# Kernel optimization log

Measured on AMD Instinct MI355X. Metric: run time of the kernel, lower is better.

## Reference

```python
import jax, jax.numpy as jnp
import numpy as np

ROUTING_ITERS = 3


def _squash(x, axis=-1):
    # sum_sq/(1+sum_sq) * x/sqrt(sum_sq), faithful to the torch squash
    sum_sq = jnp.sum(x * x, axis=axis, keepdims=True)
    return sum_sq / (1.0 + sum_sq) * x / jnp.sqrt(sum_sq)


def setup_inputs() -> dict:
    key = jax.random.key(0)
    k1, k2 = jax.random.split(key)
    B, I, O, Din, Dout = 256, 1152, 10, 8, 16
    x = jax.random.normal(k1, (B, I, Din), dtype=jnp.float32)
    W = jax.random.normal(k2, (I, O, Din, Dout), dtype=jnp.float32)
    return {"x": x, "W": W}


def reference(x, W):
    # x: [B, I, Din], W: [I, O, Din, Dout]
    I, O, Din, Dout = W.shape
    # u_hat = x @ W per (capsule_in, capsule_out): [B, I, O, Dout]
    u_hat = jnp.einsum('bid,iode->bioe', x, W)
    b = jnp.zeros((I, O), dtype=x.dtype)  # coupling logits, shared over batch
    v = None
    for _ in range(ROUTING_ITERS):
        c = jax.nn.softmax(b, axis=1)                    # softmax over out capsules
        s = jnp.einsum('bioe,io->boe', u_hat, c)         # weighted sum over in caps
        v = _squash(s, axis=-1)                          # [B, O, Dout]
        # agreement, averaged over batch (torch does .mean(dim=0))
        agree = jnp.einsum('bioe,boe->bio', u_hat, v).mean(axis=0)  # [I, O]
        b = b + agree
    # torch returns v.squeeze(1).transpose(2,3) -> [B, O, Dout, 1]
    return v[..., None]
```

## Files before the change

### kernel.cpp

```cpp
#include <hip/hip_runtime.h>
#include <math.h>

#define B    256
#define I    1152
#define O    10
#define DIN  8
#define DOUT 16
#define OE   160
#define XROW 9216
#define WROW 1280
#define PSPLIT 72
#define CHUNK  16
#define SI     8

typedef __attribute__((ext_vector_type(8))) short short8;
typedef __attribute__((ext_vector_type(4))) float floatx4;

__device__ __forceinline__ unsigned short f2bf(float f) {
    unsigned u = __builtin_bit_cast(unsigned, f);
    u += 0x7fffu + ((u >> 16) & 1u);
    return (unsigned short)(u >> 16);
}
__device__ __forceinline__ float bf2f(unsigned short h) {
    unsigned u = ((unsigned)h) << 16;
    return __builtin_bit_cast(float, u);
}

__global__ __launch_bounds__(256) void xsplit_kernel(
    const float* __restrict__ x,
    unsigned short* __restrict__ xh, unsigned short* __restrict__ xl)
{
    int g = blockIdx.x * 256 + threadIdx.x;
    float4 v = ((const float4*)x)[g];
    ushort4 h, l;
    h.x = f2bf(v.x); l.x = f2bf(v.x - bf2f(h.x));
    h.y = f2bf(v.y); l.y = f2bf(v.y - bf2f(h.y));
    h.z = f2bf(v.z); l.z = f2bf(v.z - bf2f(h.z));
    h.w = f2bf(v.w); l.w = f2bf(v.w - bf2f(h.w));
    ((ushort4*)xh)[g] = h;
    ((ushort4*)xl)[g] = l;
}

__global__ __launch_bounds__(256) void spart_mfma(
    const unsigned short* __restrict__ xh, const unsigned short* __restrict__ xl,
    const float* __restrict__ W, const float* __restrict__ c,
    float* __restrict__ sp, int first)
{
    __shared__ unsigned short Wh[80 * 64], Wl[80 * 64];
    __shared__ unsigned short Xh[128 * 64], Xl[128 * 64];

    int bid = blockIdx.x;
    int ic  = bid >> 2;
    int mb  = (bid >> 1) & 1;
    int nb  = bid & 1;
    int b0  = mb * 128;
    int oe0 = nb * 80;
    int o0  = nb * 5;
    int i0  = ic * CHUNK;

    int t    = threadIdx.x;
    int w    = t >> 6;
    int lane = t & 63;
    int l15  = lane & 15;
    int q    = lane >> 4;

    floatx4 acc[2][5];
#pragma unroll
    for (int mt = 0; mt < 2; ++mt)
#pragma unroll
        for (int nt = 0; nt < 5; ++nt) acc[mt][nt] = (floatx4)(0.f);

#pragma unroll
    for (int round = 0; round < CHUNK / SI; ++round) {
        int si0 = i0 + round * SI;
        if (round) __syncthreads();

#pragma unroll
        for (int r = 0; r < 3; ++r) {
            int p = t + 256 * r;
            if (p < 640) {
                int oeL = p % 80;
                int iL  = p / 80;
                int o   = o0 + (oeL >> 4);
                int e   = oeL & 15;
                const float* wp = W + (size_t)(si0 + iL) * WROW + o * (DIN * DOUT) + e;
                float cv = first ? 0.1f : c[(si0 + iL) * O + o];
                short8 hv, lv;
#pragma unroll
                for (int d = 0; d < 8; ++d) {
                    float wv = wp[d * DOUT] * cv;
                    unsigned short h = f2bf(wv);
                    hv[d] = (short)h;
                    lv[d] = (short)f2bf(wv - bf2f(h));
                }
                int off = oeL * 64 + ((iL ^ (oeL & 7)) << 3);
                *(short8*)(Wh + off) = hv;
                *(short8*)(Wl + off) = lv;
            }
        }
#pragma unroll
        for (int r = 0; r < 4; ++r) {
            int cg  = t + 256 * r;
            int row = cg >> 3;
            int ch  = cg & 7;
            size_t goff = (size_t)(b0 + row) * XROW + (size_t)si0 * 8 + (ch << 3);
            short8 vh = *(const short8*)(xh + goff);
            short8 vl = *(const short8*)(xl + goff);
            int off = row * 64 + ((ch ^ (row & 7)) << 3);
            *(short8*)(Xh + off) = vh;
            *(short8*)(Xl + off) = vl;
        }
        __syncthreads();

#pragma unroll
        for (int ks = 0; ks < 2; ++ks) {
            short8 ah[2], al[2];
#pragma unroll
            for (int mt = 0; mt < 2; ++mt) {
                int rm  = w * 32 + mt * 16 + l15;
                int off = rm * 64 + ((((ks << 2) + q) ^ (rm & 7)) << 3);
                ah[mt] = *(const short8*)(Xh + off);
                al[mt] = *(const short8*)(Xl + off);
            }
#pragma unroll
            for (int nt = 0; nt < 5; ++nt) {
                int rn  = nt * 16 + l15;
                int off = rn * 64 + ((((ks << 2) + q) ^ (rn & 7)) << 3);
                short8 bh = *(const short8*)(Wh + off);
                short8 bl = *(const short8*)(Wl + off);
#pragma unroll
                for (int mt = 0; mt < 2; ++mt) {
                    acc[mt][nt] = __builtin_amdgcn_mfma_f32_16x16x32_bf16(ah[mt], bh, acc[mt][nt], 0, 0, 0);
                    acc[mt][nt] = __builtin_amdgcn_mfma_f32_16x16x32_bf16(ah[mt], bl, acc[mt][nt], 0, 0, 0);
                    acc[mt][nt] = __builtin_amdgcn_mfma_f32_16x16x32_bf16(al[mt], bh, acc[mt][nt], 0, 0, 0);
                }
            }
        }
    }

    float* base = sp + (size_t)ic * (B * OE);
#pragma unroll
    for (int mt = 0; mt < 2; ++mt) {
        int row0 = b0 + w * 32 + mt * 16 + q * 4;
#pragma unroll
        for (int nt = 0; nt < 5; ++nt) {
            int col = oe0 + nt * 16 + l15;
#pragma unroll
            for (int reg = 0; reg < 4; ++reg)
                base[(row0 + reg) * OE + col] = acc[mt][nt][reg];
        }
    }
}

__global__ __launch_bounds__(256) void vred_kernel(
    const float* __restrict__ sp, float* __restrict__ dst)
{
    int g = blockIdx.x * 256 + threadIdx.x;
    float s = 0.f;
#pragma unroll 4
    for (int ic = 0; ic < PSPLIT; ++ic) s += sp[(size_t)ic * (B * OE) + g];

    float ss = s * s;
    ss += __shfl_xor(ss, 1, 16);
    ss += __shfl_xor(ss, 2, 16);
    ss += __shfl_xor(ss, 4, 16);
    ss += __shfl_xor(ss, 8, 16);
    float f = sqrtf(ss) / (1.f + ss);
    dst[g] = s * f;
}

__global__ __launch_bounds__(320) void agree_kernel(
    const float* __restrict__ x, const float* __restrict__ W,
    const float* __restrict__ v, float* __restrict__ blog,
    float* __restrict__ c, int first)
{
    int i  = blockIdx.x;
    int t  = threadIdx.x;
    int dg = (t >= OE) ? 1 : 0;
    int oe = t - dg * OE;

    __shared__ float4 Xl[B][2];
    __shared__ float  G[DIN * OE];
    __shared__ float  brow[O];

#pragma unroll
    for (int k = 0; k < 2; ++k) {
        int idx = t + 320 * k;
        if (idx < 512) {
            int r = idx >> 1;
            int h = idx & 1;
            Xl[r][h] = *(const float4*)(x + (size_t)r * XROW + i * DIN + h * 4);
        }
    }
    __syncthreads();

    float a0 = 0.f, a1 = 0.f, a2 = 0.f, a3 = 0.f;
    const float* vp = v + oe;
#pragma unroll 8
    for (int bb = 0; bb < B; ++bb) {
        float  vv = vp[bb * OE];
        float4 xq = Xl[bb][dg];
        a0 = fmaf(xq.x, vv, a0);
        a1 = fmaf(xq.y, vv, a1);
        a2 = fmaf(xq.z, vv, a2);
        a3 = fmaf(xq.w, vv, a3);
    }

    int d0 = dg * 4;
    G[(d0 + 0) * OE + oe] = a0;
    G[(d0 + 1) * OE + oe] = a1;
    G[(d0 + 2) * OE + oe] = a2;
    G[(d0 + 3) * OE + oe] = a3;
    __syncthreads();

    if (t < OE) {
        int o = t >> 4;
        const float* wr = W + (size_t)i * WROW + o * (DIN * DOUT) + (t & 15);
        float p = 0.f;
#pragma unroll
        for (int d = 0; d < DIN; ++d) p = fmaf(wr[d * DOUT], G[d * OE + t], p);
        p += __shfl_xor(p, 8, 16);
        p += __shfl_xor(p, 4, 16);
        p += __shfl_xor(p, 2, 16);
        p += __shfl_xor(p, 1, 16);
        if ((t & 15) == 0) {
            float bo = first ? 0.f : blog[i * O + o];
            bo += p * (1.f / (float)B);
            blog[i * O + o] = bo;
            brow[o] = bo;
        }
    }
    __syncthreads();

    if (t == 0) {
        float m = brow[0];
#pragma unroll
        for (int o = 1; o < O; ++o) m = fmaxf(m, brow[o]);
        float ex[O];
        float sum = 0.f;
#pragma unroll
        for (int o = 0; o < O; ++o) { ex[o] = __expf(brow[o] - m); sum += ex[o]; }
        float inv = 1.f / sum;
#pragma unroll
        for (int o = 0; o < O; ++o) c[i * O + o] = ex[o] * inv;
    }
}

extern "C" void kernel_launch(void* const* d_in, const int* in_sizes, int n_in,
                              void* d_out, int out_size, void* d_ws, size_t ws_size,
                              hipStream_t stream)
{
    const float* x = (const float*)d_in[0];
    const float* W = (const float*)d_in[1];
    float* out = (float*)d_out;

    unsigned short* xh = (unsigned short*)d_ws;
    unsigned short* xl = xh + (size_t)B * XROW;
    float* blog = (float*)(xl + (size_t)B * XROW);
    float* cbuf = blog + I * O;
    float* vbuf = cbuf + I * O;
    float* sp   = vbuf + B * OE;

    xsplit_kernel<<<(B * XROW) / (256 * 4), 256, 0, stream>>>(x, xh, xl);

    dim3 gs(4 * PSPLIT), bs(256);
    spart_mfma<<<gs, bs, 0, stream>>>(xh, xl, W, cbuf, sp, 1);
    vred_kernel<<<160, 256, 0, stream>>>(sp, vbuf);
    agree_kernel<<<I, 320, 0, stream>>>(x, W, vbuf, blog, cbuf, 1);
    spart_mfma<<<gs, bs, 0, stream>>>(xh, xl, W, cbuf, sp, 0);
    vred_kernel<<<160, 256, 0, stream>>>(sp, vbuf);
    agree_kernel<<<I, 320, 0, stream>>>(x, W, vbuf, blog, cbuf, 0);
    spart_mfma<<<gs, bs, 0, stream>>>(xh, xl, W, cbuf, sp, 0);
    vred_kernel<<<160, 256, 0, stream>>>(sp, out);
}
```

Measured before the change: 165.8 us.

## Split x into bf16 inside MFMA kernel and pre-transpose W for vector loads

Drops the separate x split kernel and its bf16 hi/lo workspace. Each wave now loads its MFMA A fragments directly from fp32 x in registers, which also removes the X shared-memory tiles. A new prep kernel transposes W once per call into an [i][oe][d] layout, so the spart and agree kernels can read 8 contiguous floats instead of strided scalars. The trade-offs are redundant x conversion across the three routing iterations and the N-split blocks, plus an extra W transpose pass. The vred loop unroll is also raised.

New measurement: 159.7 us. 1.04x faster.

```diff
diff --git a/kernel.cpp b/kernel.cpp
--- a/kernel.cpp
+++ b/kernel.cpp
@@ -13,6 +13,8 @@
 #define CHUNK  16
 #define SI     8
 
+#define WPREP_BLOCKS ((I * OE) / 256)
+
 typedef __attribute__((ext_vector_type(8))) short short8;
 typedef __attribute__((ext_vector_type(4))) float floatx4;
 
@@ -26,28 +28,43 @@
     return __builtin_bit_cast(float, u);
 }
 
-__global__ __launch_bounds__(256) void xsplit_kernel(
+__device__ __forceinline__ void split8(const float* __restrict__ xp,
+                                       short8& h8, short8& l8)
+{
+    float4 v0 = *(const float4*)xp;
+    float4 v1 = *(const float4*)(xp + 4);
+    float v[8] = {v0.x, v0.y, v0.z, v0.w, v1.x, v1.y, v1.z, v1.w};
+#pragma unroll
+    for (int d = 0; d < 8; ++d) {
+        unsigned short h = f2bf(v[d]);
+        h8[d] = (short)h;
+        l8[d] = (short)f2bf(v[d] - bf2f(h));
+    }
+}
+
+__global__ __launch_bounds__(256) void wprep_kernel(
+    const float* __restrict__ W, float* __restrict__ Wt)
+{
+    int g  = blockIdx.x * 256 + threadIdx.x;
+    int i  = g / OE;
+    int oe = g - i * OE;
+    int o  = oe >> 4;
+    int e  = oe & 15;
+    const float* wp = W + (size_t)i * WROW + o * (DIN * DOUT) + e;
+    float4 a, b;
+    a.x = wp[0 * DOUT]; a.y = wp[1 * DOUT]; a.z = wp[2 * DOUT]; a.w = wp[3 * DOUT];
+    b.x = wp[4 * DOUT]; b.y = wp[5 * DOUT]; b.z = wp[6 * DOUT]; b.w = wp[7 * DOUT];
+    float4* dst = (float4*)(Wt + (size_t)g * 8);
+    dst[0] = a;
+    dst[1] = b;
+}
+
+__global__ __launch_bounds__(256) void spart_mfma(
     const float* __restrict__ x,
-    unsigned short* __restrict__ xh, unsigned short* __restrict__ xl)
-{
-    int g = blockIdx.x * 256 + threadIdx.x;
-    float4 v = ((const float4*)x)[g];
-    ushort4 h, l;
-    h.x = f2bf(v.x); l.x = f2bf(v.x - bf2f(h.x));
-    h.y = f2bf(v.y); l.y = f2bf(v.y - bf2f(h.y));
-    h.z = f2bf(v.z); l.z = f2bf(v.z - bf2f(h.z));
-    h.w = f2bf(v.w); l.w = f2bf(v.w - bf2f(h.w));
-    ((ushort4*)xh)[g] = h;
-    ((ushort4*)xl)[g] = l;
-}
-
-__global__ __launch_bounds__(256) void spart_mfma(
-    const unsigned short* __restrict__ xh, const unsigned short* __restrict__ xl,
-    const float* __restrict__ W, const float* __restrict__ c,
+    const float* __restrict__ Wt, const float* __restrict__ c,
     float* __restrict__ sp, int first)
 {
     __shared__ unsigned short Wh[80 * 64], Wl[80 * 64];
-    __shared__ unsigned short Xh[128 * 64], Xl[128 * 64];
 
     int bid = blockIdx.x;
     int ic  = bid >> 2;
@@ -55,7 +72,6 @@
     int nb  = bid & 1;
     int b0  = mb * 128;
     int oe0 = nb * 80;
-    int o0  = nb * 5;
     int i0  = ic * CHUNK;
 
     int t    = threadIdx.x;
@@ -75,53 +91,45 @@
         int si0 = i0 + round * SI;
         if (round) __syncthreads();
 
+        short8 ah[2][2], al[2][2];
+#pragma unroll
+        for (int ks = 0; ks < 2; ++ks)
+#pragma unroll
+            for (int mt = 0; mt < 2; ++mt) {
+                const float* xp = x + (size_t)(b0 + w * 32 + mt * 16 + l15) * XROW
+                                + (size_t)si0 * 8 + (ks << 5) + (q << 3);
+                split8(xp, ah[ks][mt], al[ks][mt]);
+            }
+
 #pragma unroll
         for (int r = 0; r < 3; ++r) {
             int p = t + 256 * r;
             if (p < 640) {
                 int oeL = p % 80;
                 int iL  = p / 80;
-                int o   = o0 + (oeL >> 4);
-                int e   = oeL & 15;
-                const float* wp = W + (size_t)(si0 + iL) * WROW + o * (DIN * DOUT) + e;
+                int o   = (oe0 + oeL) >> 4;
+                const float* wp = Wt + ((size_t)(si0 + iL) * OE + oe0 + oeL) * 8;
                 float cv = first ? 0.1f : c[(si0 + iL) * O + o];
+                float4 w0 = *(const float4*)wp;
+                float4 w1 = *(const float4*)(wp + 4);
+                float wv[8] = {w0.x, w0.y, w0.z, w0.w, w1.x, w1.y, w1.z, w1.w};
                 short8 hv, lv;
 #pragma unroll
                 for (int d = 0; d < 8; ++d) {
-                    float wv = wp[d * DOUT] * cv;
-                    unsigned short h = f2bf(wv);
+                    float s = wv[d] * cv;
+                    unsigned short h = f2bf(s);
                     hv[d] = (short)h;
-                    lv[d] = (short)f2bf(wv - bf2f(h));
+                    lv[d] = (short)f2bf(s - bf2f(h));
                 }
                 int off = oeL * 64 + ((iL ^ (oeL & 7)) << 3);
                 *(short8*)(Wh + off) = hv;
                 *(short8*)(Wl + off) = lv;
             }
         }
-#pragma unroll
-        for (int r = 0; r < 4; ++r) {
-            int cg  = t + 256 * r;
-            int row = cg >> 3;
-            int ch  = cg & 7;
-            size_t goff = (size_t)(b0 + row) * XROW + (size_t)si0 * 8 + (ch << 3);
-            short8 vh = *(const short8*)(xh + goff);
-            short8 vl = *(const short8*)(xl + goff);
-            int off = row * 64 + ((ch ^ (row & 7)) << 3);
-            *(short8*)(Xh + off) = vh;
-            *(short8*)(Xl + off) = vl;
-        }
         __syncthreads();
 
 #pragma unroll
         for (int ks = 0; ks < 2; ++ks) {
-            short8 ah[2], al[2];
-#pragma unroll
-            for (int mt = 0; mt < 2; ++mt) {
-                int rm  = w * 32 + mt * 16 + l15;
-                int off = rm * 64 + ((((ks << 2) + q) ^ (rm & 7)) << 3);
-                ah[mt] = *(const short8*)(Xh + off);
-                al[mt] = *(const short8*)(Xl + off);
-            }
 #pragma unroll
             for (int nt = 0; nt < 5; ++nt) {
                 int rn  = nt * 16 + l15;
@@ -130,9 +138,9 @@
                 short8 bl = *(const short8*)(Wl + off);
 #pragma unroll
                 for (int mt = 0; mt < 2; ++mt) {
-                    acc[mt][nt] = __builtin_amdgcn_mfma_f32_16x16x32_bf16(ah[mt], bh, acc[mt][nt], 0, 0, 0);
-                    acc[mt][nt] = __builtin_amdgcn_mfma_f32_16x16x32_bf16(ah[mt], bl, acc[mt][nt], 0, 0, 0);
-                    acc[mt][nt] = __builtin_amdgcn_mfma_f32_16x16x32_bf16(al[mt], bh, acc[mt][nt], 0, 0, 0);
+                    acc[mt][nt] = __builtin_amdgcn_mfma_f32_16x16x32_bf16(ah[ks][mt], bh, acc[mt][nt], 0, 0, 0);
+                    acc[mt][nt] = __builtin_amdgcn_mfma_f32_16x16x32_bf16(ah[ks][mt], bl, acc[mt][nt], 0, 0, 0);
+                    acc[mt][nt] = __builtin_amdgcn_mfma_f32_16x16x32_bf16(al[ks][mt], bh, acc[mt][nt], 0, 0, 0);
                 }
             }
         }
@@ -157,7 +165,7 @@
 {
     int g = blockIdx.x * 256 + threadIdx.x;
     float s = 0.f;
-#pragma unroll 4
+#pragma unroll 8
     for (int ic = 0; ic < PSPLIT; ++ic) s += sp[(size_t)ic * (B * OE) + g];
 
     float ss = s * s;
@@ -170,7 +178,7 @@
 }
 
 __global__ __launch_bounds__(320) void agree_kernel(
-    const float* __restrict__ x, const float* __restrict__ W,
+    const float* __restrict__ x, const float* __restrict__ Wt,
     const float* __restrict__ v, float* __restrict__ blog,
     float* __restrict__ c, int first)
 {
@@ -215,10 +223,18 @@
 
     if (t < OE) {
         int o = t >> 4;
-        const float* wr = W + (size_t)i * WROW + o * (DIN * DOUT) + (t & 15);
+        const float* wr = Wt + ((size_t)i * OE + t) * 8;
+        float4 wa = *(const float4*)wr;
+        float4 wb = *(const float4*)(wr + 4);
         float p = 0.f;
-#pragma unroll
-        for (int d = 0; d < DIN; ++d) p = fmaf(wr[d * DOUT], G[d * OE + t], p);
+        p = fmaf(wa.x, G[0 * OE + t], p);
+        p = fmaf(wa.y, G[1 * OE + t], p);
+        p = fmaf(wa.z, G[2 * OE + t], p);
+        p = fmaf(wa.w, G[3 * OE + t], p);
+        p = fmaf(wb.x, G[4 * OE + t], p);
+        p = fmaf(wb.y, G[5 * OE + t], p);
+        p = fmaf(wb.z, G[6 * OE + t], p);
+        p = fmaf(wb.w, G[7 * OE + t], p);
         p += __shfl_xor(p, 8, 16);
         p += __shfl_xor(p, 4, 16);
         p += __shfl_xor(p, 2, 16);
@@ -254,22 +270,21 @@
     const float* W = (const float*)d_in[1];
     float* out = (float*)d_out;
 
-    unsigned short* xh = (unsigned short*)d_ws;
-    unsigned short* xl = xh + (size_t)B * XROW;
-    float* blog = (float*)(xl + (size_t)B * XROW);
+    float* blog = (float*)d_ws;
     float* cbuf = blog + I * O;
     float* vbuf = cbuf + I * O;
-    float* sp   = vbuf + B * OE;
-
-    xsplit_kernel<<<(B * XROW) / (256 * 4), 256, 0, stream>>>(x, xh, xl);
+    float* Wt   = vbuf + B * OE;
+    float* sp   = Wt + (size_t)I * OE * DIN;
+
+    wprep_kernel<<<WPREP_BLOCKS, 256, 0, stream>>>(W, Wt);
 
     dim3 gs(4 * PSPLIT), bs(256);
-    spart_mfma<<<gs, bs, 0, stream>>>(xh, xl, W, cbuf, sp, 1);
+    spart_mfma<<<gs, bs, 0, stream>>>(x, Wt, cbuf, sp, 1);
     vred_kernel<<<160, 256, 0, stream>>>(sp, vbuf);
-    agree_kernel<<<I, 320, 0, stream>>>(x, W, vbuf, blog, cbuf, 1);
-    spart_mfma<<<gs, bs, 0, stream>>>(xh, xl, W, cbuf, sp, 0);
+    agree_kernel<<<I, 320, 0, stream>>>(x, Wt, vbuf, blog, cbuf, 1);
+    spart_mfma<<<gs, bs, 0, stream>>>(x, Wt, cbuf, sp, 0);
     vred_kernel<<<160, 256, 0, stream>>>(sp, vbuf);
-    agree_kernel<<<I, 320, 0, stream>>>(x, W, vbuf, blog, cbuf, 0);
-    spart_mfma<<<gs, bs, 0, stream>>>(xh, xl, W, cbuf, sp, 0);
+    agree_kernel<<<I, 320, 0, stream>>>(x, Wt, vbuf, blog, cbuf, 0);
+    spart_mfma<<<gs, bs, 0, stream>>>(x, Wt, cbuf, sp, 0);
     vred_kernel<<<160, 256, 0, stream>>>(sp, out);
 }
```
